# Kernel optimization log

Measured on AMD Instinct MI355X. Metric: run time of the kernel, lower is better.

The kernel has to match this reference:

```python
import jax, jax.numpy as jnp
import numpy as np

REALSHAPE = (32, 256, 256)   # even dims required
SHAPE = (32, 256, 129)       # rfft half-spectrum shape
MIDS = (16, 128, 128)
KCUT = 4
B, C = 4, 3


def _hs_np(f):
    # numpy mirror of Fourier.hermitian_symmetric (used only to build the constant feed mask)
    m0, m1, m2 = MIDS
    f = f.copy()
    f[m0+1:, 0, 0] = f[1:m0, 0, 0][::-1].conj()
    f[m0+1:, 0, m2] = f[1:m0, 0, m2][::-1].conj()
    f[m0+1:, m1, 0] = f[1:m0, m1, 0][::-1].conj()
    f[m0+1:, m1, m2] = f[1:m0, m1, m2][::-1].conj()
    f[0, m1+1:, 0] = f[0, 1:m1, 0][::-1].conj()
    f[0, m1+1:, m2] = f[0, 1:m1, m2][::-1].conj()
    f[m0, m1+1:, 0] = f[m0, 1:m1, 0][::-1].conj()
    f[m0, m1+1:, m2] = f[m0, 1:m1, m2][::-1].conj()
    f[m0+1:, m1+1:, 0] = f[1:m0, 1:m1, 0][::-1, ::-1].conj()
    f[m0+1:, 1:m1, 0] = f[1:m0, m1+1:, 0][::-1, ::-1].conj()
    f[m0+1:, m1+1:, m2] = f[1:m0, 1:m1, m2][::-1, ::-1].conj()
    f[m0+1:, 1:m1, m2] = f[1:m0, m1+1:, m2][::-1, ::-1].conj()
    return f


def _constants():
    ks = [np.fft.fftfreq(d, 1.0 / d) for d in SHAPE[:-1]] + [np.arange(SHAPE[-1])]
    kgrid = np.array(np.meshgrid(*ks, indexing='ij'))
    ksq = np.sum(kgrid ** 2, axis=0)
    holders = np.stack(np.meshgrid(*[np.arange(d) for d in SHAPE], indexing='ij'))
    same = np.all(np.stack([_hs_np(h) for h in holders]) == holders, axis=0)
    rem = same & (ksq <= KCUT ** 2)
    feed = np.stack([rem, rem.copy()])
    m0, m1, m2 = MIDS
    for idx in [(0, 0, 0), (0, 0, m2), (0, m1, 0), (0, m1, m2),
                (m0, 0, 0), (m0, 0, m2), (m0, m1, 0), (m0, m1, m2)]:
        feed[(1,) + idx] = False  # purely real corner modes
    feed_idx = np.nonzero(feed.reshape(-1))[0].astype(np.int32)
    ks_sel = np.stack([ksq, ksq])[feed]  # dimscale = (1,1,1)
    Pk = (1.0 / (ks_sel + 1.0) * float(np.prod(REALSHAPE))).astype(np.float32)
    grid = np.stack(np.meshgrid(*[np.arange(d) for d in REALSHAPE], indexing='ij')).astype(np.float32)
    return feed_idx, Pk, grid


def setup_inputs() -> dict:
    feed_idx, Pk, grid = _constants()
    key = jax.random.key(0)
    k1, k2 = jax.random.split(key)
    fr = jax.random.normal(k1, (B, C) + REALSHAPE, jnp.float32)
    seeds = jax.random.normal(k2, (1, 3 * feed_idx.size), jnp.float32)
    return {
        'fr': fr,
        'seeds': seeds,
        'Pk': jnp.asarray(Pk),
        'defscale': jnp.ones(3, jnp.float32),  # defscale / dimscale
        'grid': jnp.asarray(grid),
        'feed_idx': jnp.asarray(feed_idx),
    }


def _hs(f):
    # jax hermitian-symmetrize the rfft half-spectrum (writes are non-overlapping with reads)
    m0, m1, m2 = MIDS
    fl = lambda a: jnp.flip(a, 0).conj()
    fl2 = lambda a: jnp.flip(a, (0, 1)).conj()
    f = f.at[m0+1:, 0, 0].set(fl(f[1:m0, 0, 0]))
    f = f.at[m0+1:, 0, m2].set(fl(f[1:m0, 0, m2]))
    f = f.at[m0+1:, m1, 0].set(fl(f[1:m0, m1, 0]))
    f = f.at[m0+1:, m1, m2].set(fl(f[1:m0, m1, m2]))
    f = f.at[0, m1+1:, 0].set(fl(f[0, 1:m1, 0]))
    f = f.at[0, m1+1:, m2].set(fl(f[0, 1:m1, m2]))
    f = f.at[m0, m1+1:, 0].set(fl(f[m0, 1:m1, 0]))
    f = f.at[m0, m1+1:, m2].set(fl(f[m0, 1:m1, m2]))
    f = f.at[m0+1:, m1+1:, 0].set(fl2(f[1:m0, 1:m1, 0]))
    f = f.at[m0+1:, 1:m1, 0].set(fl2(f[1:m0, m1+1:, 0]))
    f = f.at[m0+1:, m1+1:, m2].set(fl2(f[1:m0, 1:m1, m2]))
    f = f.at[m0+1:, 1:m1, m2].set(fl2(f[1:m0, m1+1:, m2]))
    return f


def _forward(fr, seeds, Pk, defscale, grid, feed_idx):
    fdim = feed_idx.shape[0]
    # scale sparse coefficients by the power spectrum
    x = seeds.reshape(3, fdim) * Pk[None, :] * defscale[:, None]
    # scatter into the (2, *SHAPE) re/im spectrum via flat indices
    nfull = 2 * int(np.prod(SHAPE))
    arr = jnp.zeros((3, nfull), jnp.float32).at[:, feed_idx].set(x).reshape(3, 2, *SHAPE)
    comp = (arr[:, 0] + 1j * arr[:, 1]).astype(jnp.complex64)
    comp = jax.vmap(_hs)(comp)
    disp = jnp.fft.irfftn(comp[None], s=REALSHAPE, axes=(2, 3, 4))  # (1,3,D,H,W) float32
    D, H, W = REALSHAPE
    norm = (jnp.asarray(REALSHAPE, jnp.float32) - 1.0)[None, :, None, None, None]
    moved = 2.0 * ((grid[None] - disp) / norm) - 1.0  # normalized coords in [-1,1]
    gz, gy, gx = moved[0, 0], moved[0, 1], moved[0, 2]  # torch grid channel order [2,1,0] -> (x=W, y=H, z=D)
    # grid_sample: bilinear, padding_mode='border' (clamp float coords), align_corners=True
    fz = jnp.clip((gz + 1.0) * 0.5 * (D - 1), 0.0, D - 1)
    fy = jnp.clip((gy + 1.0) * 0.5 * (H - 1), 0.0, H - 1)
    fx = jnp.clip((gx + 1.0) * 0.5 * (W - 1), 0.0, W - 1)
    z0 = jnp.floor(fz); y0 = jnp.floor(fy); x0 = jnp.floor(fx)
    wz = fz - z0; wy = fy - y0; wx = fx - x0  # (D,H,W), broadcast against (B,C,D,H,W)
    z0i = z0.astype(jnp.int32); z1i = jnp.minimum(z0i + 1, D - 1)
    y0i = y0.astype(jnp.int32); y1i = jnp.minimum(y0i + 1, H - 1)
    x0i = x0.astype(jnp.int32); x1i = jnp.minimum(x0i + 1, W - 1)
    g = lambda zi, yi, xi: fr[:, :, zi, yi, xi]  # gather -> (B,C,D,H,W)
    c00 = g(z0i, y0i, x0i) * (1 - wx) + g(z0i, y0i, x1i) * wx
    c01 = g(z0i, y1i, x0i) * (1 - wx) + g(z0i, y1i, x1i) * wx
    c10 = g(z1i, y0i, x0i) * (1 - wx) + g(z1i, y0i, x1i) * wx
    c11 = g(z1i, y1i, x0i) * (1 - wx) + g(z1i, y1i, x1i) * wx
    c0 = c00 * (1 - wy) + c01 * wy
    c1 = c10 * (1 - wy) + c11 * wy
    return c0 * (1 - wz) + c1 * wz


def reference(fr, seeds, Pk, defscale, grid, feed_idx):
    return _forward(fr, seeds, Pk, defscale, grid, feed_idx)
```

## Files before the change

kernel.cpp:

```cpp
#include <hip/hip_runtime.h>
#include <math.h>

#define D0 32
#define D1 256
#define D2 256
#define HS2 129
#define NVOX (D0*D1*D2)
#define KMAX 4
#define NK 9
#define NK2 5
#define NCH 3
#define BATCH 4
#define FCH 3
#define NBC (BATCH*FCH)
#define C_FLOATS (NCH*NK*NK*NK2*2)

__global__ __launch_bounds__(256) void build_S(
    const float* __restrict__ seeds, const float* __restrict__ Pk,
    const float* __restrict__ defscale, const int* __restrict__ feed_idx,
    int fdim, float* __restrict__ S)
{
    __shared__ float C[C_FLOATS];
    __shared__ int fed[NK*NK];
    int t = threadIdx.x;
    for (int i = t; i < C_FLOATS; i += 256) C[i] = 0.0f;
    if (t < NK*NK) fed[t] = 0;
    __syncthreads();
    float ds0 = defscale[0], ds1 = defscale[1], ds2 = defscale[2];
    const int STR_RI = D0 * D1 * HS2;
    const int STR_A  = D1 * HS2;
    for (int j = t; j < fdim; j += 256) {
        int idx = feed_idx[j];
        int ri = idx / STR_RI; int r = idx - ri * STR_RI;
        int a  = r / STR_A;    r -= a * STR_A;
        int b  = r / HS2;      int c = r - b * HS2;
        int k0 = (a < D0/2) ? a : a - D0;
        int k1 = (b < D1/2) ? b : b - D1;
        if (k0 < -KMAX || k0 > KMAX || k1 < -KMAX || k1 > KMAX || c > KMAX) continue;
        int i0 = k0 + KMAX, i1 = k1 + KMAX;
        float pk = Pk[j];
        int base = ((i0*NK + i1)*NK2 + c)*2 + ri;
        C[base]                 = seeds[0*fdim + j] * pk * ds0;
        C[base + 1*NK*NK*NK2*2] = seeds[1*fdim + j] * pk * ds1;
        C[base + 2*NK*NK*NK2*2] = seeds[2*fdim + j] * pk * ds2;
        if (c == 0) fed[i0*NK + i1] = 1;
    }
    __syncthreads();
    if (t < NK*NK && !fed[t]) {
        int i0 = t / NK, i1 = t - i0*NK;
        int m0 = (NK-1) - i0, m1 = (NK-1) - i1;
        for (int ch = 0; ch < NCH; ++ch) {
            int dst = ((ch*NK*NK + i0*NK + i1)*NK2 + 0)*2;
            int src = ((ch*NK*NK + m0*NK + m1)*NK2 + 0)*2;
            C[dst]   = C[src];
            C[dst+1] = -C[src+1];
        }
    }
    __syncthreads();

    int zyl = t >> 3;
    int g   = t & 7;
    int zy = blockIdx.x * 32 + zyl;
    int z = zy >> 8, y = zy & 255;

    float w0r[NK], w0i[NK], w1r[NK], w1i[NK];
    {
        float th = (float)z * (6.28318530717958647692f / (float)D0);
        float sb, cb; __sincosf(th, &sb, &cb);
        w0r[KMAX] = 1.0f; w0i[KMAX] = 0.0f;
        float pr = 1.0f, pi = 0.0f;
        #pragma unroll
        for (int k = 1; k <= KMAX; ++k) {
            float nr = pr*cb - pi*sb, ni = pr*sb + pi*cb;
            pr = nr; pi = ni;
            w0r[KMAX+k] = pr; w0i[KMAX+k] = pi;
            w0r[KMAX-k] = pr; w0i[KMAX-k] = -pi;
        }
    }
    {
        float th = (float)y * (6.28318530717958647692f / (float)D1);
        float sb, cb; __sincosf(th, &sb, &cb);
        w1r[KMAX] = 1.0f; w1i[KMAX] = 0.0f;
        float pr = 1.0f, pi = 0.0f;
        #pragma unroll
        for (int k = 1; k <= KMAX; ++k) {
            float nr = pr*cb - pi*sb, ni = pr*sb + pi*cb;
            pr = nr; pi = ni;
            w1r[KMAX+k] = pr; w1i[KMAX+k] = pi;
            w1r[KMAX-k] = pr; w1i[KMAX-k] = -pi;
        }
    }

    float Sr[NCH*NK2], Si[NCH*NK2];
    #pragma unroll
    for (int i = 0; i < NCH*NK2; ++i) { Sr[i] = 0.0f; Si[i] = 0.0f; }

    for (int m = g; m < NK*NK; m += 8) {
        int i0 = m / NK, i1 = m - i0*NK;
        float Tr = w0r[i0]*w1r[i1] - w0i[i0]*w1i[i1];
        float Ti = w0r[i0]*w1i[i1] + w0i[i0]*w1r[i1];
        const float* Cp = C + m*NK2*2;
        #pragma unroll
        for (int ch = 0; ch < NCH; ++ch) {
            #pragma unroll
            for (int k2 = 0; k2 < NK2; ++k2) {
                float cr = Cp[ch*(NK*NK*NK2*2) + k2*2];
                float ci = Cp[ch*(NK*NK*NK2*2) + k2*2 + 1];
                int o = ch*NK2 + k2;
                Sr[o] += cr*Tr - ci*Ti;
                Si[o] += cr*Ti + ci*Tr;
            }
        }
    }

    #pragma unroll
    for (int off = 4; off >= 1; off >>= 1) {
        #pragma unroll
        for (int i = 0; i < NCH*NK2; ++i) {
            Sr[i] += __shfl_down(Sr[i], off, 8);
            Si[i] += __shfl_down(Si[i], off, 8);
        }
    }

    if (g == 0) {
        const float invN = 1.0f / (float)NVOX;
        #pragma unroll
        for (int ch = 0; ch < NCH; ++ch) {
            #pragma unroll
            for (int k2 = 0; k2 < NK2; ++k2) {
                int o = ch*NK2 + k2;
                float sc = (k2 == 0) ? invN : 2.0f*invN;
                S[(o*2 + 0)*8192 + zy] = Sr[o] * sc;
                S[(o*2 + 1)*8192 + zy] = Si[o] * sc;
            }
        }
    }
}

__global__ __launch_bounds__(256) void deform_sample(
    const float* __restrict__ fr, const float* __restrict__ S,
    float* __restrict__ out)
{
    int i = blockIdx.x;
    int u = i & 7;
    int b  = u >> 1;
    int zh = u & 1;
    int j = i >> 3;
    int z = (zh << 4) + (j >> 8);
    int y = j & 255;
    int zy = (z << 8) + y;
    int x = threadIdx.x;

    float s0r[NCH], skr[NCH][KMAX], ski[NCH][KMAX];
    #pragma unroll
    for (int ch = 0; ch < NCH; ++ch) {
        s0r[ch] = S[((ch*NK2 + 0)*2 + 0)*8192 + zy];
        #pragma unroll
        for (int k = 1; k <= KMAX; ++k) {
            skr[ch][k-1] = S[((ch*NK2 + k)*2 + 0)*8192 + zy];
            ski[ch][k-1] = S[((ch*NK2 + k)*2 + 1)*8192 + zy];
        }
    }

    float th = (float)x * (6.28318530717958647692f / (float)D2);
    float sb, cb; __sincosf(th, &sb, &cb);
    float ckr[KMAX], cks[KMAX];
    ckr[0] = cb; cks[0] = sb;
    #pragma unroll
    for (int k = 1; k < KMAX; ++k) {
        float nr = ckr[k-1]*cb - cks[k-1]*sb;
        float ni = cks[k-1]*cb + ckr[k-1]*sb;
        ckr[k] = nr; cks[k] = ni;
    }

    float d[NCH];
    #pragma unroll
    for (int ch = 0; ch < NCH; ++ch) {
        float acc = s0r[ch];
        #pragma unroll
        for (int k = 0; k < KMAX; ++k)
            acc += skr[ch][k]*ckr[k] - ski[ch][k]*cks[k];
        d[ch] = acc;
    }

    float fz = fminf(fmaxf((float)z - d[0], 0.0f), (float)(D0-1));
    float fy = fminf(fmaxf((float)y - d[1], 0.0f), (float)(D1-1));
    float fx = fminf(fmaxf((float)x - d[2], 0.0f), (float)(D2-1));

    float z0f = floorf(fz), y0f = floorf(fy), x0f = floorf(fx);
    int z0 = (int)z0f, y0 = (int)y0f, x0 = (int)x0f;
    int z1 = min(z0 + 1, D0-1), y1 = min(y0 + 1, D1-1), x1 = min(x0 + 1, D2-1);
    float wz = fz - z0f, wy = fy - y0f, wx = fx - x0f;
    float wz0 = 1.0f - wz, wy0 = 1.0f - wy, wx0 = 1.0f - wx;

    int o00 = (z0 << 16) + (y0 << 8);
    int o01 = (z0 << 16) + (y1 << 8);
    int o10 = (z1 << 16) + (y0 << 8);
    int o11 = (z1 << 16) + (y1 << 8);

    const float* __restrict__ v0p = fr + ((size_t)(b*3 + 0) << 21);
    const float* __restrict__ v1p = fr + ((size_t)(b*3 + 1) << 21);
    const float* __restrict__ v2p = fr + ((size_t)(b*3 + 2) << 21);
    size_t ob = ((size_t)(b*3) << 21) + (zy << 8) + x;

    #pragma unroll
    for (int c = 0; c < 3; ++c) {
        const float* __restrict__ v = (c == 0) ? v0p : (c == 1) ? v1p : v2p;
        float c00 = v[o00 + x0]*wx0 + v[o00 + x1]*wx;
        float c01 = v[o01 + x0]*wx0 + v[o01 + x1]*wx;
        float c10 = v[o10 + x0]*wx0 + v[o10 + x1]*wx;
        float c11 = v[o11 + x0]*wx0 + v[o11 + x1]*wx;
        float cc0 = c00*wy0 + c01*wy;
        float cc1 = c10*wy0 + c11*wy;
        __builtin_nontemporal_store(cc0*wz0 + cc1*wz, &out[ob + ((size_t)c << 21)]);
    }
}

extern "C" void kernel_launch(void* const* d_in, const int* in_sizes, int n_in,
                              void* d_out, int out_size, void* d_ws, size_t ws_size,
                              hipStream_t stream) {
    const float* fr       = (const float*)d_in[0];
    const float* seeds    = (const float*)d_in[1];
    const float* Pk       = (const float*)d_in[2];
    const float* defscale = (const float*)d_in[3];
    const int*   feed_idx = (const int*)d_in[5];
    int fdim = in_sizes[2];

    float* S = (float*)d_ws;

    build_S<<<256, 256, 0, stream>>>(seeds, Pk, defscale, feed_idx, fdim, S);
    deform_sample<<<8192*4, 256, 0, stream>>>(fr, S, (float*)d_out);
}
```

Before: 311.5 us.

## Use interleaved per-row S layout and paired-float corner gathers in sampler

build_S now writes the 30 spectral coefficients for each (z,y) row contiguously, with a stride of 32 floats, instead of as separate planes, so deform_sample reads them from one small contiguous region. The sampler fetches each x-neighbour pair with a single 8-byte load, clamping the left index to W-2 and selecting the value at the border. It also hoists all 12 loads ahead of the lerps and rewrites the interpolation in lerp form. The intent is to halve the gather instruction count and make the S loads contiguous. The cost is that the 8-byte loads can be misaligned when xm is odd, and the lerp form can change rounding slightly.

```diff
diff --git a/kernel.cpp b/kernel.cpp
--- a/kernel.cpp
+++ b/kernel.cpp
@@ -14,6 +14,8 @@
 #define FCH 3
 #define NBC (BATCH*FCH)
 #define C_FLOATS (NCH*NK*NK*NK2*2)
+
+typedef float v2f __attribute__((ext_vector_type(2)));
 
 __global__ __launch_bounds__(256) void build_S(
     const float* __restrict__ seeds, const float* __restrict__ Pk,
@@ -124,14 +126,15 @@
 
     if (g == 0) {
         const float invN = 1.0f / (float)NVOX;
+        float* Sp = S + (size_t)zy * 32;
         #pragma unroll
         for (int ch = 0; ch < NCH; ++ch) {
             #pragma unroll
             for (int k2 = 0; k2 < NK2; ++k2) {
                 int o = ch*NK2 + k2;
                 float sc = (k2 == 0) ? invN : 2.0f*invN;
-                S[(o*2 + 0)*8192 + zy] = Sr[o] * sc;
-                S[(o*2 + 1)*8192 + zy] = Si[o] * sc;
+                Sp[ch*10 + k2*2 + 0] = Sr[o] * sc;
+                Sp[ch*10 + k2*2 + 1] = Si[o] * sc;
             }
         }
     }
@@ -151,16 +154,10 @@
     int zy = (z << 8) + y;
     int x = threadIdx.x;
 
-    float s0r[NCH], skr[NCH][KMAX], ski[NCH][KMAX];
-    #pragma unroll
-    for (int ch = 0; ch < NCH; ++ch) {
-        s0r[ch] = S[((ch*NK2 + 0)*2 + 0)*8192 + zy];
-        #pragma unroll
-        for (int k = 1; k <= KMAX; ++k) {
-            skr[ch][k-1] = S[((ch*NK2 + k)*2 + 0)*8192 + zy];
-            ski[ch][k-1] = S[((ch*NK2 + k)*2 + 1)*8192 + zy];
-        }
-    }
+    const float* __restrict__ Sp = S + (size_t)zy * 32;
+    float s[30];
+    #pragma unroll
+    for (int q = 0; q < 30; ++q) s[q] = Sp[q];
 
     float th = (float)x * (6.28318530717958647692f / (float)D2);
     float sb, cb; __sincosf(th, &sb, &cb);
@@ -176,10 +173,10 @@
     float d[NCH];
     #pragma unroll
     for (int ch = 0; ch < NCH; ++ch) {
-        float acc = s0r[ch];
-        #pragma unroll
-        for (int k = 0; k < KMAX; ++k)
-            acc += skr[ch][k]*ckr[k] - ski[ch][k]*cks[k];
+        float acc = s[ch*10 + 0];
+        #pragma unroll
+        for (int k = 1; k <= KMAX; ++k)
+            acc += s[ch*10 + k*2]*ckr[k-1] - s[ch*10 + k*2 + 1]*cks[k-1];
         d[ch] = acc;
     }
 
@@ -189,30 +186,42 @@
 
     float z0f = floorf(fz), y0f = floorf(fy), x0f = floorf(fx);
     int z0 = (int)z0f, y0 = (int)y0f, x0 = (int)x0f;
-    int z1 = min(z0 + 1, D0-1), y1 = min(y0 + 1, D1-1), x1 = min(x0 + 1, D2-1);
+    int z1 = min(z0 + 1, D0-1), y1 = min(y0 + 1, D1-1);
     float wz = fz - z0f, wy = fy - y0f, wx = fx - x0f;
-    float wz0 = 1.0f - wz, wy0 = 1.0f - wy, wx0 = 1.0f - wx;
-
-    int o00 = (z0 << 16) + (y0 << 8);
-    int o01 = (z0 << 16) + (y1 << 8);
-    int o10 = (z1 << 16) + (y0 << 8);
-    int o11 = (z1 << 16) + (y1 << 8);
-
-    const float* __restrict__ v0p = fr + ((size_t)(b*3 + 0) << 21);
-    const float* __restrict__ v1p = fr + ((size_t)(b*3 + 1) << 21);
-    const float* __restrict__ v2p = fr + ((size_t)(b*3 + 2) << 21);
-    size_t ob = ((size_t)(b*3) << 21) + (zy << 8) + x;
-
-    #pragma unroll
-    for (int c = 0; c < 3; ++c) {
-        const float* __restrict__ v = (c == 0) ? v0p : (c == 1) ? v1p : v2p;
-        float c00 = v[o00 + x0]*wx0 + v[o00 + x1]*wx;
-        float c01 = v[o01 + x0]*wx0 + v[o01 + x1]*wx;
-        float c10 = v[o10 + x0]*wx0 + v[o10 + x1]*wx;
-        float c11 = v[o11 + x0]*wx0 + v[o11 + x1]*wx;
-        float cc0 = c00*wy0 + c01*wy;
-        float cc1 = c10*wy0 + c11*wy;
-        __builtin_nontemporal_store(cc0*wz0 + cc1*wz, &out[ob + ((size_t)c << 21)]);
+
+    int xm = min(x0, D2-2);
+    bool hi = (x0 > xm);
+
+    int o00 = (z0 << 16) + (y0 << 8) + xm;
+    int o01 = (z0 << 16) + (y1 << 8) + xm;
+    int o10 = (z1 << 16) + (y0 << 8) + xm;
+    int o11 = (z1 << 16) + (y1 << 8) + xm;
+
+    v2f P[FCH][4];
+    #pragma unroll
+    for (int c = 0; c < FCH; ++c) {
+        const float* __restrict__ v = fr + ((size_t)(b*FCH + c) << 21);
+        P[c][0] = *(const v2f*)(v + o00);
+        P[c][1] = *(const v2f*)(v + o01);
+        P[c][2] = *(const v2f*)(v + o10);
+        P[c][3] = *(const v2f*)(v + o11);
+    }
+
+    size_t ob = ((size_t)(b*FCH) << 21) + ((size_t)zy << 8) + x;
+    #pragma unroll
+    for (int c = 0; c < FCH; ++c) {
+        float a00 = hi ? P[c][0].y : P[c][0].x;
+        float a01 = hi ? P[c][1].y : P[c][1].x;
+        float a10 = hi ? P[c][2].y : P[c][2].x;
+        float a11 = hi ? P[c][3].y : P[c][3].x;
+        float c00 = a00 + wx * (P[c][0].y - a00);
+        float c01 = a01 + wx * (P[c][1].y - a01);
+        float c10 = a10 + wx * (P[c][2].y - a10);
+        float c11 = a11 + wx * (P[c][3].y - a11);
+        float c0 = c00 + wy * (c01 - c00);
+        float c1 = c10 + wy * (c11 - c10);
+        __builtin_nontemporal_store(c0 + wz * (c1 - c0),
+                                    &out[ob + ((size_t)c << 21)]);
     }
 }
 
```

Result: faster. 281.4 us (-9.7%).
